# Kernel optimization log

Hardware: AMD Instinct MI355X
Metric: run time of the kernel (lower is better)

Reference implementation:

```python
import jax, jax.numpy as jnp
import numpy as np

N, E, F_IN, HID, EPS = 50000, 800000, 128, 256, 1e-5

def _glorot(key, shape):
    scale = 1.0 / np.sqrt(shape[0])
    return jax.random.uniform(key, shape, jnp.float32, -scale, scale)

def setup_inputs() -> dict:
    key = jax.random.key(0)
    ks = jax.random.split(key, 20)
    x = jax.random.normal(ks[0], (N, F_IN), jnp.float32)
    edge_index = jax.random.randint(ks[1], (2, E), 0, N, jnp.int64)
    inp = {"x": x, "edge_index": edge_index}
    dims = [F_IN, HID, HID]
    for i in range(3):
        d_in = dims[i]
        inp[f"Wn{i}"] = _glorot(ks[2 + 4 * i], (d_in, HID))      # lin_l weight (neighbors), with bias
        inp[f"bn{i}"] = jnp.zeros((HID,), jnp.float32)
        inp[f"Wr{i}"] = _glorot(ks[3 + 4 * i], (d_in, HID))      # lin_r weight (root), no bias
        inp[f"g{i}"] = jnp.ones((HID,), jnp.float32)              # BN gamma
        inp[f"b{i}"] = jnp.zeros((HID,), jnp.float32)             # BN beta
    return inp

def _sage_bn_elu(x, src, dst, Wn, bn, Wr, g, b):
    # mean aggregation of source features onto destination nodes
    agg = jax.ops.segment_sum(x[src], dst, num_segments=N)                      # [N, d_in]
    deg = jax.ops.segment_sum(jnp.ones((src.shape[0],), x.dtype), dst, num_segments=N)
    agg = agg / jnp.maximum(deg, 1.0)[:, None]
    h = agg @ Wn + bn + x @ Wr                                                  # SAGEConv(root_weight=True)
    mu = jnp.mean(h, axis=0)
    var = jnp.mean((h - mu) ** 2, axis=0)                                       # biased var (BN training)
    h = (h - mu) * jax.lax.rsqrt(var + EPS) * g + b
    return jnp.where(h > 0, h, jnp.expm1(h))                                    # ELU(alpha=1)

def reference(x, edge_index, Wn0, bn0, Wr0, g0, b0, Wn1, bn1, Wr1, g1, b1, Wn2, bn2, Wr2, g2, b2):
    src, dst = edge_index[0], edge_index[1]
    h = _sage_bn_elu(x, src, dst, Wn0, bn0, Wr0, g0, b0)
    h = _sage_bn_elu(h, src, dst, Wn1, bn1, Wr1, g1, b1)
    h = _sage_bn_elu(h, src, dst, Wn2, bn2, Wr2, g2, b2)
    return h
```

## Files before the change

kernel.cpp:

```cpp
#include <hip/hip_runtime.h>
#include <math.h>

#define N_NODES 50000
#define N_EDGES 800000
#define F_IN    128
#define HID     256
#define BN_EPS  1e-5f
#define SCAN_BLOCKS ((N_NODES + 255) / 256)
#define RB256       ((N_NODES + 255) / 256)

typedef unsigned int uint;
typedef __attribute__((ext_vector_type(8))) short bf16x8;
typedef __attribute__((ext_vector_type(4))) float f32x4;

__device__ __forceinline__ float bf2f(unsigned short u) {
    return __uint_as_float((uint)u << 16);
}
__device__ __forceinline__ unsigned short f2bf(float f) {
    uint u = __float_as_uint(f);
    return (unsigned short)((u + 0x7FFFu + ((u >> 16) & 1u)) >> 16);
}

__device__ __forceinline__ void gload16(const unsigned short* g, unsigned short* l) {
    __builtin_amdgcn_global_load_lds(
        (const __attribute__((address_space(1))) void*)g,
        (__attribute__((address_space(3))) void*)l, 16, 0, 0);
}

__device__ __forceinline__ void acc_u4(float* a, uint4 v) {
    a[0] += bf2f((unsigned short)(v.x & 0xFFFF)); a[1] += bf2f((unsigned short)(v.x >> 16));
    a[2] += bf2f((unsigned short)(v.y & 0xFFFF)); a[3] += bf2f((unsigned short)(v.y >> 16));
    a[4] += bf2f((unsigned short)(v.z & 0xFFFF)); a[5] += bf2f((unsigned short)(v.z >> 16));
    a[6] += bf2f((unsigned short)(v.w & 0xFFFF)); a[7] += bf2f((unsigned short)(v.w >> 16));
}
__device__ __forceinline__ void acc_u4m(float* a, uint4 v, float m) {
    a[0] += m * bf2f((unsigned short)(v.x & 0xFFFF)); a[1] += m * bf2f((unsigned short)(v.x >> 16));
    a[2] += m * bf2f((unsigned short)(v.y & 0xFFFF)); a[3] += m * bf2f((unsigned short)(v.y >> 16));
    a[4] += m * bf2f((unsigned short)(v.z & 0xFFFF)); a[5] += m * bf2f((unsigned short)(v.z >> 16));
    a[6] += m * bf2f((unsigned short)(v.w & 0xFFFF)); a[7] += m * bf2f((unsigned short)(v.w >> 16));
}

__global__ void hist_kernel(const int* __restrict__ dst, int* __restrict__ deg) {
    int e = blockIdx.x * blockDim.x + threadIdx.x;
    if (e < N_EDGES) atomicAdd(&deg[dst[e]], 1);
}

__global__ __launch_bounds__(256) void scan1_kernel(const int* __restrict__ deg,
                                                    int* __restrict__ row_ptr,
                                                    int* __restrict__ partials) {
    __shared__ int sm[256];
    int i = blockIdx.x * 256 + threadIdx.x;
    int v = (i < N_NODES) ? deg[i] : 0;
    sm[threadIdx.x] = v;
    __syncthreads();
    for (int off = 1; off < 256; off <<= 1) {
        int t = (threadIdx.x >= off) ? sm[threadIdx.x - off] : 0;
        __syncthreads();
        sm[threadIdx.x] += t;
        __syncthreads();
    }
    if (i < N_NODES) row_ptr[i] = sm[threadIdx.x] - v;
    if (threadIdx.x == 255) partials[blockIdx.x] = sm[255];
}

__global__ __launch_bounds__(256) void scan2_kernel(int* __restrict__ partials) {
    __shared__ int sm[256];
    int t = threadIdx.x;
    int v = (t < SCAN_BLOCKS) ? partials[t] : 0;
    sm[t] = v;
    __syncthreads();
    for (int off = 1; off < 256; off <<= 1) {
        int p = (t >= off) ? sm[t - off] : 0;
        __syncthreads();
        sm[t] += p;
        __syncthreads();
    }
    if (t < SCAN_BLOCKS) partials[t] = sm[t] - v;
}

__global__ __launch_bounds__(256) void scan3_kernel(int* __restrict__ row_ptr,
                                                    int* __restrict__ cursor,
                                                    const int* __restrict__ partials) {
    int i = blockIdx.x * 256 + threadIdx.x;
    if (i < N_NODES) {
        int v = row_ptr[i] + partials[blockIdx.x];
        row_ptr[i] = v;
        cursor[i]  = v;
    }
    if (i == 0) row_ptr[N_NODES] = N_EDGES;
}

__global__ void fill_kernel(const int* __restrict__ src, const int* __restrict__ dst,
                            int* __restrict__ cursor, int* __restrict__ csr_src) {
    int e = blockIdx.x * blockDim.x + threadIdx.x;
    if (e >= N_EDGES) return;
    int pos = atomicAdd(&cursor[dst[e]], 1);
    csr_src[pos] = src[e];
}

__global__ void cast_bf16_kernel(const float* __restrict__ x, unsigned short* __restrict__ xb,
                                 int total4) {
    int i = blockIdx.x * blockDim.x + threadIdx.x;
    if (i >= total4) return;
    float4 v = *(const float4*)&x[(long)i * 4];
    unsigned short o[4] = {f2bf(v.x), f2bf(v.y), f2bf(v.z), f2bf(v.w)};
    *(uint2*)&xb[(long)i * 4] = *(const uint2*)o;
}

__global__ __launch_bounds__(256) void wt_kernel(const float* __restrict__ Wn,
                                                 const float* __restrict__ Wr,
                                                 int K1, int KT, unsigned short* __restrict__ WT) {
    int n  = threadIdx.x;
    int k0 = blockIdx.x * 16;
    unsigned short o[16];
#pragma unroll
    for (int j = 0; j < 16; ++j) {
        int k = k0 + j;
        float v = (k < K1) ? Wn[k * HID + n] : Wr[(k - K1) * HID + n];
        o[j] = f2bf(v);
    }
    *(uint4*)&WT[(long)n * KT + k0]     = *(const uint4*)&o[0];
    *(uint4*)&WT[(long)n * KT + k0 + 8] = *(const uint4*)&o[8];
}

template<int D>
__global__ __launch_bounds__(256) void gather_mean_kernel(
    const unsigned short* __restrict__ x, const int* __restrict__ row_ptr,
    const int* __restrict__ csr_src, unsigned short* __restrict__ agg) {
    int node = blockIdx.x * 4 + (threadIdx.x >> 6);
    int lane = threadIdx.x & 63;
    if (node >= N_NODES) return;
    int beg = row_ptr[node], end = row_ptr[node + 1];
    float acc[8];
#pragma unroll
    for (int j = 0; j < 8; j++) acc[j] = 0.f;
    int e = beg;

    if constexpr (D == 256) {
        const int half = lane >> 5;
        const long lo  = (long)(lane & 31) * 8;
        for (; e + 8 <= end; e += 8) {
            int s0 = csr_src[e + half],     s1 = csr_src[e + 2 + half];
            int s2 = csr_src[e + 4 + half], s3 = csr_src[e + 6 + half];
            uint4 v0 = *(const uint4*)&x[(long)s0 * 256 + lo];
            uint4 v1 = *(const uint4*)&x[(long)s1 * 256 + lo];
            uint4 v2 = *(const uint4*)&x[(long)s2 * 256 + lo];
            uint4 v3 = *(const uint4*)&x[(long)s3 * 256 + lo];
            acc_u4(acc, v0); acc_u4(acc, v1); acc_u4(acc, v2); acc_u4(acc, v3);
        }
        for (; e + 2 <= end; e += 2) {
            int s0 = csr_src[e + half];
            uint4 v0 = *(const uint4*)&x[(long)s0 * 256 + lo];
            acc_u4(acc, v0);
        }
        if (e < end) {
            int s0 = csr_src[e];
            uint4 v0 = *(const uint4*)&x[(long)s0 * 256 + lo];
            acc_u4m(acc, v0, (half == 0) ? 1.f : 0.f);
        }
#pragma unroll
        for (int j = 0; j < 8; j++) acc[j] += __shfl_xor(acc[j], 32);
        float inv = 1.0f / fmaxf((float)(end - beg), 1.0f);
        if (half == 0) {
            unsigned short ov[8];
#pragma unroll
            for (int j = 0; j < 8; j++) ov[j] = f2bf(acc[j] * inv);
            *(uint4*)&agg[(long)node * 256 + lo] = *(const uint4*)ov;
        }
    } else {
        const int grp = lane >> 4;
        const long lo = (long)(lane & 15) * 8;
        for (; e + 8 <= end; e += 8) {
            int sA = csr_src[e + grp], sB = csr_src[e + 4 + grp];
            uint4 vA = *(const uint4*)&x[(long)sA * 128 + lo];
            uint4 vB = *(const uint4*)&x[(long)sB * 128 + lo];
            acc_u4(acc, vA); acc_u4(acc, vB);
        }
        for (; e + 4 <= end; e += 4) {
            int sA = csr_src[e + grp];
            uint4 vA = *(const uint4*)&x[(long)sA * 128 + lo];
            acc_u4(acc, vA);
        }
        for (; e < end; e++) {
            int s0 = csr_src[e];
            uint4 v0 = *(const uint4*)&x[(long)s0 * 128 + lo];
            acc_u4m(acc, v0, (grp == 0) ? 1.f : 0.f);
        }
#pragma unroll
        for (int j = 0; j < 8; j++) {
            acc[j] += __shfl_xor(acc[j], 32);
            acc[j] += __shfl_xor(acc[j], 16);
        }
        float inv = 1.0f / fmaxf((float)(end - beg), 1.0f);
        if (lane < 16) {
            unsigned short ov[8];
#pragma unroll
            for (int j = 0; j < 8; j++) ov[j] = f2bf(acc[j] * inv);
            *(uint4*)&agg[(long)node * 128 + lo] = *(const uint4*)ov;
        }
    }
}

template<int K1, int K2>
__global__ __launch_bounds__(512) void mfma_gemm_kernel(
    const unsigned short* __restrict__ A1, const unsigned short* __restrict__ A2,
    const unsigned short* __restrict__ WT, const float* __restrict__ bias,
    unsigned short* __restrict__ Hout, float* __restrict__ sred) {
    constexpr int KT = K1 + K2;
    constexpr int NITER = KT / 64;
    __shared__ unsigned short As[2][256 * 64];
    __shared__ unsigned short Bs[2][256 * 64];

    const int tid  = threadIdx.x;
    const int wave = tid >> 6;
    const int lane = tid & 63;
    const int m16  = lane & 15;
    const int quad = lane >> 4;
    const int WR   = wave >> 2;
    const int WC   = wave & 3;
    const int r0   = blockIdx.x * 256;
    const int rl = lane >> 3;
    const int cl = lane & 7;
    const int csw = cl ^ rl;

    f32x4 acc[8][4];
#pragma unroll
    for (int mt = 0; mt < 8; mt++)
#pragma unroll
        for (int nt = 0; nt < 4; nt++) acc[mt][nt] = (f32x4){0.f, 0.f, 0.f, 0.f};

    auto issue = [&](int t) {
        const int buf = t & 1;
        const int k0  = t * 64;
        const unsigned short* Ab;
        int pitch, kk;
        if (k0 < K1) { Ab = A1; pitch = K1; kk = k0; }
        else         { Ab = A2; pitch = K2; kk = k0 - K1; }
#pragma unroll
        for (int j = 0; j < 4; ++j) {
            int lr = wave * 32 + j * 8 + rl;
            long gr = min(r0 + lr, N_NODES - 1);
            gload16(&Ab[gr * pitch + kk + csw * 8], &As[buf][(wave * 32 + j * 8) * 64]);
        }
#pragma unroll
        for (int j = 0; j < 4; ++j) {
            long gn = wave * 32 + j * 8 + rl;
            gload16(&WT[gn * KT + k0 + csw * 8], &Bs[buf][(wave * 32 + j * 8) * 64]);
        }
    };

    issue(0);

#pragma unroll
    for (int it = 0; it < NITER; ++it) {
        const int cur = it & 1;
        if (it + 1 < NITER) {
            issue(it + 1);
            asm volatile("s_waitcnt vmcnt(8)" ::: "memory");
        } else {
            asm volatile("s_waitcnt vmcnt(0)" ::: "memory");
        }
        __builtin_amdgcn_s_barrier();
#pragma unroll
        for (int ks = 0; ks < 2; ++ks) {
            bf16x8 afrag[8], bfrag[4];
#pragma unroll
            for (int mt = 0; mt < 8; mt++) {
                int ar = WR * 128 + mt * 16 + m16;
                afrag[mt] = *(const bf16x8*)&As[cur][ar * 64 + (((ks * 4 + quad) ^ (m16 & 7)) * 8)];
            }
#pragma unroll
            for (int nt = 0; nt < 4; nt++) {
                int br = WC * 64 + nt * 16 + m16;
                bfrag[nt] = *(const bf16x8*)&Bs[cur][br * 64 + (((ks * 4 + quad) ^ (m16 & 7)) * 8)];
            }
#pragma unroll
            for (int mt = 0; mt < 8; mt++)
#pragma unroll
                for (int nt = 0; nt < 4; nt++)
                    acc[mt][nt] = __builtin_amdgcn_mfma_f32_16x16x32_bf16(
                        afrag[mt], bfrag[nt], acc[mt][nt], 0, 0, 0);
        }
        __builtin_amdgcn_s_barrier();
    }

#pragma unroll
    for (int nt = 0; nt < 4; nt++) {
        int lcol = WC * 64 + nt * 16 + m16;
        float bv = bias[lcol];
        float s = 0.f, q = 0.f;
#pragma unroll
        for (int mt = 0; mt < 8; mt++) {
#pragma unroll
            for (int reg = 0; reg < 4; reg++) {
                int row = r0 + WR * 128 + mt * 16 + quad * 4 + reg;
                float v = acc[mt][nt][reg] + bv;
                if (row < N_NODES) {
                    Hout[(long)row * HID + lcol] = f2bf(v);
                    s += v;
                    q += v * v;
                }
            }
        }
        s += __shfl_xor(s, 16); s += __shfl_xor(s, 32);
        q += __shfl_xor(q, 16); q += __shfl_xor(q, 32);
        if (quad == 0) {
            float* base = &sred[(long)(blockIdx.x * 2 + WR) * 512];
            base[lcol]       = s;
            base[256 + lcol] = q;
        }
    }
}

__global__ __launch_bounds__(512) void bn_reduce_kernel(const float* __restrict__ sred,
                                                        const float* __restrict__ g,
                                                        const float* __restrict__ b,
                                                        float* __restrict__ ss, int nrows) {
    __shared__ float qsm[256];
    int t  = threadIdx.x;
    int ch = t & 255;
    int off = (t < 256) ? 0 : 256;
    float S0 = 0.f, S1 = 0.f, S2 = 0.f, S3 = 0.f;
    int rb = 0;
    for (; rb + 4 <= nrows; rb += 4) {
        S0 += sred[(long)(rb + 0) * 512 + off + ch];
        S1 += sred[(long)(rb + 1) * 512 + off + ch];
        S2 += sred[(long)(rb + 2) * 512 + off + ch];
        S3 += sred[(long)(rb + 3) * 512 + off + ch];
    }
    for (; rb < nrows; rb++) S0 += sred[(long)rb * 512 + off + ch];
    float Sv = (S0 + S1) + (S2 + S3);
    if (t >= 256) qsm[ch] = Sv;
    __syncthreads();
    if (t < 256) {
        float mu  = Sv * (1.0f / N_NODES);
        float var = qsm[ch] * (1.0f / N_NODES) - mu * mu;
        var = fmaxf(var, 0.f);
        float sc = rsqrtf(var + BN_EPS) * g[ch];
        ss[ch]       = sc;
        ss[HID + ch] = b[ch] - mu * sc;
    }
}

template<bool OUT32>
__global__ void bn_elu_kernel(const unsigned short* __restrict__ h, const float* __restrict__ ss,
                              void* __restrict__ out) {
    const int total4 = N_NODES * HID / 4;
    int i = blockIdx.x * blockDim.x + threadIdx.x;
    if (i >= total4) return;
    int c4 = (i % (HID / 4)) * 4;
    uint2 v = *(const uint2*)&h[(long)i * 4];
    float4 sc = *(const float4*)&ss[c4];
    float4 sh = *(const float4*)&ss[HID + c4];
    float in[4] = {bf2f((unsigned short)(v.x & 0xFFFF)), bf2f((unsigned short)(v.x >> 16)),
                   bf2f((unsigned short)(v.y & 0xFFFF)), bf2f((unsigned short)(v.y >> 16))};
    float scv[4] = {sc.x, sc.y, sc.z, sc.w};
    float shv[4] = {sh.x, sh.y, sh.z, sh.w};
    float o[4];
#pragma unroll
    for (int j = 0; j < 4; j++) {
        float t = fmaf(in[j], scv[j], shv[j]);
        o[j] = t > 0.f ? t : expm1f(t);
    }
    if (OUT32) {
        float4 ov = {o[0], o[1], o[2], o[3]};
        *(float4*)&((float*)out)[(long)i * 4] = ov;
    } else {
        unsigned short ov[4] = {f2bf(o[0]), f2bf(o[1]), f2bf(o[2]), f2bf(o[3])};
        *(uint2*)&((unsigned short*)out)[(long)i * 4] = *(const uint2*)ov;
    }
}

extern "C" void kernel_launch(void* const* d_in, const int* in_sizes, int n_in,
                              void* d_out, int out_size, void* d_ws, size_t ws_size,
                              hipStream_t stream) {
    const float* x   = (const float*)d_in[0];
    const int*   ei  = (const int*)d_in[1];
    const int*   src = ei;
    const int*   dst = ei + N_EDGES;
    const float* Wn[3] = {(const float*)d_in[2],  (const float*)d_in[7],  (const float*)d_in[12]};
    const float* bn[3] = {(const float*)d_in[3],  (const float*)d_in[8],  (const float*)d_in[13]};
    const float* Wr[3] = {(const float*)d_in[4],  (const float*)d_in[9],  (const float*)d_in[14]};
    const float* g [3] = {(const float*)d_in[5],  (const float*)d_in[10], (const float*)d_in[15]};
    const float* b [3] = {(const float*)d_in[6],  (const float*)d_in[11], (const float*)d_in[16]};
    float* out = (float*)d_out;

    const size_t BF = (size_t)N_NODES * HID * 2;
    char* ws = (char*)d_ws;
    unsigned short* B0  = (unsigned short*)(ws);
    unsigned short* B1  = (unsigned short*)(ws + BF);
    unsigned short* B2  = (unsigned short*)(ws + 2 * BF);
    unsigned short* XB  = (unsigned short*)(ws + 3 * BF);
    char* ws2 = ws + 3 * BF + (size_t)N_NODES * F_IN * 2;
    unsigned short* WT0 = (unsigned short*)(ws2);
    unsigned short* WT1 = (unsigned short*)(ws2 + 256 * 256 * 2);
    unsigned short* WT2 = (unsigned short*)(ws2 + 256 * 256 * 2 + 256 * 512 * 2);
    char* ws3 = ws2 + 256 * 256 * 2 + 2 * (256 * 512 * 2);
    int*   row_ptr = (int*)ws3;
    int*   cursor  = row_ptr + (N_NODES + 1);
    int*   deg_i   = cursor + N_NODES;
    int*   partial = deg_i + N_NODES;
    int*   csr_src = partial + SCAN_BLOCKS;
    float* sred    = (float*)(csr_src + N_EDGES);
    float* ss      = sred + (size_t)2 * RB256 * 512;

    const int eb = (N_EDGES + 255) / 256;
    const int gather_blocks = (N_NODES + 3) / 4;
    const int elu_blocks = (N_NODES * HID / 4 + 255) / 256;

    hipMemsetAsync(deg_i, 0, N_NODES * sizeof(int), stream);
    hist_kernel<<<eb, 256, 0, stream>>>(dst, deg_i);
    scan1_kernel<<<SCAN_BLOCKS, 256, 0, stream>>>(deg_i, row_ptr, partial);
    scan2_kernel<<<1, 256, 0, stream>>>(partial);
    scan3_kernel<<<SCAN_BLOCKS, 256, 0, stream>>>(row_ptr, cursor, partial);
    fill_kernel<<<eb, 256, 0, stream>>>(src, dst, cursor, csr_src);
    cast_bf16_kernel<<<(N_NODES * F_IN / 4 + 255) / 256, 256, 0, stream>>>(x, XB, N_NODES * F_IN / 4);
    wt_kernel<<<(2 * F_IN) / 16, 256, 0, stream>>>(Wn[0], Wr[0], F_IN, 2 * F_IN, WT0);
    wt_kernel<<<(2 * HID) / 16, 256, 0, stream>>>(Wn[1], Wr[1], HID, 2 * HID, WT1);
    wt_kernel<<<(2 * HID) / 16, 256, 0, stream>>>(Wn[2], Wr[2], HID, 2 * HID, WT2);

    gather_mean_kernel<F_IN><<<gather_blocks, 256, 0, stream>>>(XB, row_ptr, csr_src, B0);
    mfma_gemm_kernel<F_IN, F_IN><<<RB256, 512, 0, stream>>>(B0, XB, WT0, bn[0], B1, sred);
    bn_reduce_kernel<<<1, 512, 0, stream>>>(sred, g[0], b[0], ss, 2 * RB256);
    bn_elu_kernel<false><<<elu_blocks, 256, 0, stream>>>(B1, ss, B2);

    gather_mean_kernel<HID><<<gather_blocks, 256, 0, stream>>>(B2, row_ptr, csr_src, B0);
    mfma_gemm_kernel<HID, HID><<<RB256, 512, 0, stream>>>(B0, B2, WT1, bn[1], B1, sred);
    bn_reduce_kernel<<<1, 512, 0, stream>>>(sred, g[1], b[1], ss, 2 * RB256);
    bn_elu_kernel<false><<<elu_blocks, 256, 0, stream>>>(B1, ss, B2);

    gather_mean_kernel<HID><<<gather_blocks, 256, 0, stream>>>(B2, row_ptr, csr_src, B0);
    mfma_gemm_kernel<HID, HID><<<RB256, 512, 0, stream>>>(B0, B2, WT2, bn[2], B1, sred);
    bn_reduce_kernel<<<1, 512, 0, stream>>>(sred, g[2], b[2], ss, 2 * RB256);
    bn_elu_kernel<true><<<elu_blocks, 256, 0, stream>>>(B1, ss, out);
}
```

Before: 578.0 us.

## Fuse GEMM, BatchNorm reduction and ELU via cooperative grid sync; deepen gather unroll

The GEMM becomes a cooperative kernel that keeps its accumulators in registers. After writing per-block column sums it waits on a grid-wide sync, then every block reduces the BN statistics itself and applies scale, shift and ELU before writing the activation directly. This removes the bf16 intermediate H write and re-read, plus two kernel launches per layer. The gather kernel gets an extra 16-edge unrolled loop for more memory-level parallelism, and the CSR fill uses nontemporal stores. The cost is that all 196 blocks must be co-resident, and every block redundantly rereads the full partial-sum array.

```diff
diff --git a/kernel.cpp b/kernel.cpp
--- a/kernel.cpp
+++ b/kernel.cpp
@@ -1,5 +1,8 @@
 #include <hip/hip_runtime.h>
+#include <hip/hip_cooperative_groups.h>
 #include <math.h>
+
+namespace cg = cooperative_groups;
 
 #define N_NODES 50000
 #define N_EDGES 800000
@@ -95,7 +98,7 @@
     int e = blockIdx.x * blockDim.x + threadIdx.x;
     if (e >= N_EDGES) return;
     int pos = atomicAdd(&cursor[dst[e]], 1);
-    csr_src[pos] = src[e];
+    __builtin_nontemporal_store(src[e], &csr_src[pos]);
 }
 
 __global__ void cast_bf16_kernel(const float* __restrict__ x, unsigned short* __restrict__ xb,
@@ -139,6 +142,22 @@
     if constexpr (D == 256) {
         const int half = lane >> 5;
         const long lo  = (long)(lane & 31) * 8;
+        for (; e + 16 <= end; e += 16) {
+            int s0 = csr_src[e + half],      s1 = csr_src[e + 2 + half];
+            int s2 = csr_src[e + 4 + half],  s3 = csr_src[e + 6 + half];
+            int s4 = csr_src[e + 8 + half],  s5 = csr_src[e + 10 + half];
+            int s6 = csr_src[e + 12 + half], s7 = csr_src[e + 14 + half];
+            uint4 v0 = *(const uint4*)&x[(long)s0 * 256 + lo];
+            uint4 v1 = *(const uint4*)&x[(long)s1 * 256 + lo];
+            uint4 v2 = *(const uint4*)&x[(long)s2 * 256 + lo];
+            uint4 v3 = *(const uint4*)&x[(long)s3 * 256 + lo];
+            uint4 v4 = *(const uint4*)&x[(long)s4 * 256 + lo];
+            uint4 v5 = *(const uint4*)&x[(long)s5 * 256 + lo];
+            uint4 v6 = *(const uint4*)&x[(long)s6 * 256 + lo];
+            uint4 v7 = *(const uint4*)&x[(long)s7 * 256 + lo];
+            acc_u4(acc, v0); acc_u4(acc, v1); acc_u4(acc, v2); acc_u4(acc, v3);
+            acc_u4(acc, v4); acc_u4(acc, v5); acc_u4(acc, v6); acc_u4(acc, v7);
+        }
         for (; e + 8 <= end; e += 8) {
             int s0 = csr_src[e + half],     s1 = csr_src[e + 2 + half];
             int s2 = csr_src[e + 4 + half], s3 = csr_src[e + 6 + half];
@@ -170,6 +189,15 @@
     } else {
         const int grp = lane >> 4;
         const long lo = (long)(lane & 15) * 8;
+        for (; e + 16 <= end; e += 16) {
+            int sA = csr_src[e + grp],     sB = csr_src[e + 4 + grp];
+            int sC = csr_src[e + 8 + grp], sD = csr_src[e + 12 + grp];
+            uint4 vA = *(const uint4*)&x[(long)sA * 128 + lo];
+            uint4 vB = *(const uint4*)&x[(long)sB * 128 + lo];
+            uint4 vC = *(const uint4*)&x[(long)sC * 128 + lo];
+            uint4 vD = *(const uint4*)&x[(long)sD * 128 + lo];
+            acc_u4(acc, vA); acc_u4(acc, vB); acc_u4(acc, vC); acc_u4(acc, vD);
+        }
         for (; e + 8 <= end; e += 8) {
             int sA = csr_src[e + grp], sB = csr_src[e + 4 + grp];
             uint4 vA = *(const uint4*)&x[(long)sA * 128 + lo];
@@ -201,15 +229,18 @@
     }
 }
 
-template<int K1, int K2>
-__global__ __launch_bounds__(512) void mfma_gemm_kernel(
+template<int K1, int K2, bool OUT32>
+__global__ __launch_bounds__(512) void mfma_gemm_fused(
     const unsigned short* __restrict__ A1, const unsigned short* __restrict__ A2,
     const unsigned short* __restrict__ WT, const float* __restrict__ bias,
-    unsigned short* __restrict__ Hout, float* __restrict__ sred) {
+    const float* __restrict__ gam, const float* __restrict__ bet,
+    void* __restrict__ actout, float* __restrict__ sred) {
     constexpr int KT = K1 + K2;
     constexpr int NITER = KT / 64;
+    constexpr int NROWS = 2 * RB256;
     __shared__ unsigned short As[2][256 * 64];
     __shared__ unsigned short Bs[2][256 * 64];
+    __shared__ float ssm[512];
 
     const int tid  = threadIdx.x;
     const int wave = tid >> 6;
@@ -295,11 +326,8 @@
             for (int reg = 0; reg < 4; reg++) {
                 int row = r0 + WR * 128 + mt * 16 + quad * 4 + reg;
                 float v = acc[mt][nt][reg] + bv;
-                if (row < N_NODES) {
-                    Hout[(long)row * HID + lcol] = f2bf(v);
-                    s += v;
-                    q += v * v;
-                }
+                acc[mt][nt][reg] = v;
+                if (row < N_NODES) { s += v; q += v * v; }
             }
         }
         s += __shfl_xor(s, 16); s += __shfl_xor(s, 32);
@@ -310,64 +338,49 @@
             base[256 + lcol] = q;
         }
     }
-}
-
-__global__ __launch_bounds__(512) void bn_reduce_kernel(const float* __restrict__ sred,
-                                                        const float* __restrict__ g,
-                                                        const float* __restrict__ b,
-                                                        float* __restrict__ ss, int nrows) {
-    __shared__ float qsm[256];
-    int t  = threadIdx.x;
-    int ch = t & 255;
-    int off = (t < 256) ? 0 : 256;
-    float S0 = 0.f, S1 = 0.f, S2 = 0.f, S3 = 0.f;
-    int rb = 0;
-    for (; rb + 4 <= nrows; rb += 4) {
-        S0 += sred[(long)(rb + 0) * 512 + off + ch];
-        S1 += sred[(long)(rb + 1) * 512 + off + ch];
-        S2 += sred[(long)(rb + 2) * 512 + off + ch];
-        S3 += sred[(long)(rb + 3) * 512 + off + ch];
-    }
-    for (; rb < nrows; rb++) S0 += sred[(long)rb * 512 + off + ch];
-    float Sv = (S0 + S1) + (S2 + S3);
-    if (t >= 256) qsm[ch] = Sv;
+
+    cg::this_grid().sync();
+
+    {
+        float S0 = 0.f, S1 = 0.f, S2 = 0.f, S3 = 0.f;
+#pragma unroll 1
+        for (int rb = 0; rb < NROWS; rb += 4) {
+            S0 += sred[(long)(rb + 0) * 512 + tid];
+            S1 += sred[(long)(rb + 1) * 512 + tid];
+            S2 += sred[(long)(rb + 2) * 512 + tid];
+            S3 += sred[(long)(rb + 3) * 512 + tid];
+        }
+        ssm[tid] = (S0 + S1) + (S2 + S3);
+    }
     __syncthreads();
-    if (t < 256) {
-        float mu  = Sv * (1.0f / N_NODES);
-        float var = qsm[ch] * (1.0f / N_NODES) - mu * mu;
+    if (tid < 256) {
+        float mu  = ssm[tid] * (1.0f / N_NODES);
+        float var = ssm[256 + tid] * (1.0f / N_NODES) - mu * mu;
         var = fmaxf(var, 0.f);
-        float sc = rsqrtf(var + BN_EPS) * g[ch];
-        ss[ch]       = sc;
-        ss[HID + ch] = b[ch] - mu * sc;
-    }
-}
-
-template<bool OUT32>
-__global__ void bn_elu_kernel(const unsigned short* __restrict__ h, const float* __restrict__ ss,
-                              void* __restrict__ out) {
-    const int total4 = N_NODES * HID / 4;
-    int i = blockIdx.x * blockDim.x + threadIdx.x;
-    if (i >= total4) return;
-    int c4 = (i % (HID / 4)) * 4;
-    uint2 v = *(const uint2*)&h[(long)i * 4];
-    float4 sc = *(const float4*)&ss[c4];
-    float4 sh = *(const float4*)&ss[HID + c4];
-    float in[4] = {bf2f((unsigned short)(v.x & 0xFFFF)), bf2f((unsigned short)(v.x >> 16)),
-                   bf2f((unsigned short)(v.y & 0xFFFF)), bf2f((unsigned short)(v.y >> 16))};
-    float scv[4] = {sc.x, sc.y, sc.z, sc.w};
-    float shv[4] = {sh.x, sh.y, sh.z, sh.w};
-    float o[4];
-#pragma unroll
-    for (int j = 0; j < 4; j++) {
-        float t = fmaf(in[j], scv[j], shv[j]);
-        o[j] = t > 0.f ? t : expm1f(t);
-    }
-    if (OUT32) {
-        float4 ov = {o[0], o[1], o[2], o[3]};
-        *(float4*)&((float*)out)[(long)i * 4] = ov;
-    } else {
-        unsigned short ov[4] = {f2bf(o[0]), f2bf(o[1]), f2bf(o[2]), f2bf(o[3])};
-        *(uint2*)&((unsigned short*)out)[(long)i * 4] = *(const uint2*)ov;
+        float sc = rsqrtf(var + BN_EPS) * gam[tid];
+        ssm[tid]       = sc;
+        ssm[256 + tid] = bet[tid] - mu * sc;
+    }
+    __syncthreads();
+
+#pragma unroll
+    for (int nt = 0; nt < 4; nt++) {
+        int lcol = WC * 64 + nt * 16 + m16;
+        float sc = ssm[lcol];
+        float sh = ssm[256 + lcol];
+#pragma unroll
+        for (int mt = 0; mt < 8; mt++) {
+#pragma unroll
+            for (int reg = 0; reg < 4; reg++) {
+                int row = r0 + WR * 128 + mt * 16 + quad * 4 + reg;
+                if (row < N_NODES) {
+                    float t = fmaf(acc[mt][nt][reg], sc, sh);
+                    float o = t > 0.f ? t : expm1f(t);
+                    if (OUT32) ((float*)actout)[(long)row * HID + lcol] = o;
+                    else       ((unsigned short*)actout)[(long)row * HID + lcol] = f2bf(o);
+                }
+            }
+        }
     }
 }
 
@@ -402,11 +415,9 @@
     int*   partial = deg_i + N_NODES;
     int*   csr_src = partial + SCAN_BLOCKS;
     float* sred    = (float*)(csr_src + N_EDGES);
-    float* ss      = sred + (size_t)2 * RB256 * 512;
 
     const int eb = (N_EDGES + 255) / 256;
     const int gather_blocks = (N_NODES + 3) / 4;
-    const int elu_blocks = (N_NODES * HID / 4 + 255) / 256;
 
     hipMemsetAsync(deg_i, 0, N_NODES * sizeof(int), stream);
     hist_kernel<<<eb, 256, 0, stream>>>(dst, deg_i);
@@ -420,17 +431,32 @@
     wt_kernel<<<(2 * HID) / 16, 256, 0, stream>>>(Wn[2], Wr[2], HID, 2 * HID, WT2);
 
     gather_mean_kernel<F_IN><<<gather_blocks, 256, 0, stream>>>(XB, row_ptr, csr_src, B0);
-    mfma_gemm_kernel<F_IN, F_IN><<<RB256, 512, 0, stream>>>(B0, XB, WT0, bn[0], B1, sred);
-    bn_reduce_kernel<<<1, 512, 0, stream>>>(sred, g[0], b[0], ss, 2 * RB256);
-    bn_elu_kernel<false><<<elu_blocks, 256, 0, stream>>>(B1, ss, B2);
+    {
+        const unsigned short* a1 = B0; const unsigned short* a2 = XB; const unsigned short* wt = WT0;
+        const float* bi = bn[0]; const float* gg = g[0]; const float* bb = b[0];
+        void* ao = (void*)B2; float* sr = sred;
+        void* args[8] = {&a1, &a2, &wt, &bi, &gg, &bb, &ao, &sr};
+        hipLaunchCooperativeKernel(reinterpret_cast<const void*>(&mfma_gemm_fused<F_IN, F_IN, false>),
+                                   dim3(RB256), dim3(512), args, 0, stream);
+    }
 
     gather_mean_kernel<HID><<<gather_blocks, 256, 0, stream>>>(B2, row_ptr, csr_src, B0);
-    mfma_gemm_kernel<HID, HID><<<RB256, 512, 0, stream>>>(B0, B2, WT1, bn[1], B1, sred);
-    bn_reduce_kernel<<<1, 512, 0, stream>>>(sred, g[1], b[1], ss, 2 * RB256);
-    bn_elu_kernel<false><<<elu_blocks, 256, 0, stream>>>(B1, ss, B2);
+    {
+        const unsigned short* a1 = B0; const unsigned short* a2 = B2; const unsigned short* wt = WT1;
+        const float* bi = bn[1]; const float* gg = g[1]; const float* bb = b[1];
+        void* ao = (void*)B2; float* sr = sred;
+        void* args[8] = {&a1, &a2, &wt, &bi, &gg, &bb, &ao, &sr};
+        hipLaunchCooperativeKernel(reinterpret_cast<const void*>(&mfma_gemm_fused<HID, HID, false>),
+                                   dim3(RB256), dim3(512), args, 0, stream);
+    }
 
     gather_mean_kernel<HID><<<gather_blocks, 256, 0, stream>>>(B2, row_ptr, csr_src, B0);
-    mfma_gemm_kernel<HID, HID><<<RB256, 512, 0, stream>>>(B0, B2, WT2, bn[2], B1, sred);
-    bn_reduce_kernel<<<1, 512, 0, stream>>>(sred, g[2], b[2], ss, 2 * RB256);
-    bn_elu_kernel<true><<<elu_blocks, 256, 0, stream>>>(B1, ss, out);
-}
+    {
+        const unsigned short* a1 = B0; const unsigned short* a2 = B2; const unsigned short* wt = WT2;
+        const float* bi = bn[2]; const float* gg = g[2]; const float* bb = b[2];
+        void* ao = (void*)out; float* sr = sred;
+        void* args[8] = {&a1, &a2, &wt, &bi, &gg, &bb, &ao, &sr};
+        hipLaunchCooperativeKernel(reinterpret_cast<const void*>(&mfma_gemm_fused<HID, HID, true>),
+                                   dim3(RB256), dim3(512), args, 0, stream);
+    }
+}
```

Measured after the change: 697.6 us. 1.21x slower.
